# Performance work log

Measured on AMD Instinct MI355X. Metric: run time of the kernel, lower is better.

## Reference

```python
import jax, jax.numpy as jnp
import numpy as np

H, B, T, DH = 16, 2, 2048, 64
MODEL_DIM = 1024


def setup_inputs() -> dict:
    key = jax.random.key(0)
    ks = jax.random.split(key, 5)
    q = jax.random.normal(ks[0], (H, B, T, DH), dtype=jnp.float32)
    k = jax.random.normal(ks[1], (H, B, T, DH), dtype=jnp.float32)
    v = jax.random.normal(ks[2], (H, B, T, DH), dtype=jnp.float32)
    Wo_w = jax.random.normal(ks[3], (MODEL_DIM, H * DH), dtype=jnp.float32) * 0.02
    Wo_b = jax.random.normal(ks[4], (MODEL_DIM,), dtype=jnp.float32) * 0.02
    return {"q": q, "k": k, "v": v, "Wo_w": Wo_w, "Wo_b": Wo_b}


def reference(q, k, v, Wo_w, Wo_b):
    # per-head scaled dot-product attention; scale uses per-head dk (=DH)
    scale = jnp.sqrt(jnp.asarray(DH, dtype=q.dtype))
    # scores: [H, B, T, T]
    scores = jnp.einsum('hbtd,hbsd->hbts', q, k) / scale
    # causal mask (additive -1e12 on strict upper triangle, matching torch code)
    mask = jnp.triu(jnp.ones((T, T), dtype=bool), 1)
    scores = scores + (-1e12) * mask.astype(scores.dtype)
    weights = jax.nn.softmax(scores, axis=-1)
    # context per head: [H, B, T, DH]
    context = jnp.einsum('hbts,hbsd->hbtd', weights, v)
    # concat heads along feature dim: [B, T, H*DH]
    context = jnp.transpose(context, (1, 2, 0, 3)).reshape(B, T, H * DH)
    # output projection (torch Linear: x @ W.T + b)
    return context @ Wo_w.T + Wo_b
```

## Files before the change

kernel.cpp:

```cpp
#include <hip/hip_runtime.h>

typedef __attribute__((ext_vector_type(8))) short bf16x8;
typedef __attribute__((ext_vector_type(4))) float f32x4;
typedef __attribute__((ext_vector_type(4))) unsigned int u32x4;
typedef __attribute__((ext_vector_type(4))) unsigned short u16x4;

#define H_ 16
#define B_ 2
#define T_ 2048
#define DH_ 64
#define MD_ 1024

static __device__ inline unsigned short f2bf(float f) {
    union { float f; unsigned u; } x; x.f = f;
    unsigned r = (x.u + 0x7fffu + ((x.u >> 16) & 1u)) >> 16;
    return (unsigned short)r;
}
static __device__ inline unsigned int pack_bf2(float lo, float hi) {
    return __builtin_amdgcn_perm(__float_as_uint(hi), __float_as_uint(lo), 0x07060302u);
}
static __device__ inline unsigned short hi16(float f) {
    return (unsigned short)(__float_as_uint(f) >> 16);
}

__global__ __launch_bounds__(256) void prep_k(const float* __restrict__ k,
                                              const float* __restrict__ v,
                                              const float* __restrict__ w,
                                              unsigned short* __restrict__ kb,
                                              unsigned short* __restrict__ vtb,
                                              unsigned short* __restrict__ wob) {
    __shared__ __attribute__((aligned(16))) unsigned short vt64[64][64];
    const int blk = blockIdx.x;
    const int tid = threadIdx.x;
    if (blk < 1024) {
        int i = (blk * 256 + tid) * 4;
        f32x4 x = *(const f32x4*)(w + i);
        u16x4 y;
        y[0] = f2bf(x[0]); y[1] = f2bf(x[1]); y[2] = f2bf(x[2]); y[3] = f2bf(x[3]);
        *(u16x4*)(wob + i) = y;
    } else if (blk < 2048) {
        int j = blk - 1024;
        const int hb = j >> 5, s0 = (j & 31) * 64;
        const int row = tid >> 2, c = (tid & 3) * 16;
        const long off = (long)hb * (T_ * DH_) + (long)(s0 + row) * DH_ + c;
        const float* p = k + off;
        f32x4 a0 = *(const f32x4*)p;
        f32x4 a1 = *(const f32x4*)(p + 4);
        f32x4 a2 = *(const f32x4*)(p + 8);
        f32x4 a3 = *(const f32x4*)(p + 12);
        u32x4 w0, w1;
        w0[0] = pack_bf2(a0[0], a0[1]); w0[1] = pack_bf2(a0[2], a0[3]);
        w0[2] = pack_bf2(a1[0], a1[1]); w0[3] = pack_bf2(a1[2], a1[3]);
        w1[0] = pack_bf2(a2[0], a2[1]); w1[1] = pack_bf2(a2[2], a2[3]);
        w1[2] = pack_bf2(a3[0], a3[1]); w1[3] = pack_bf2(a3[2], a3[3]);
        *(u32x4*)(kb + off) = w0;
        *(u32x4*)(kb + off + 8) = w1;
    } else {
        int j = blk - 2048;
        const int hb = j >> 5, s0 = (j & 31) * 64;
        const int vkp = tid & 31, vdg = tid >> 5;
        const float* vp = v + (long)hb * (T_ * DH_) + (long)(s0 + 2 * vkp) * DH_ + vdg * 8;
        f32x4 va0 = *(const f32x4*)vp;
        f32x4 va1 = *(const f32x4*)(vp + 4);
        f32x4 vb0 = *(const f32x4*)(vp + DH_);
        f32x4 vb1 = *(const f32x4*)(vp + DH_ + 4);
#pragma unroll
        for (int jj = 0; jj < 4; jj++) {
            ((unsigned int*)&vt64[vdg * 8 + jj][0])[vkp]     = pack_bf2(va0[jj], vb0[jj]);
            ((unsigned int*)&vt64[vdg * 8 + 4 + jj][0])[vkp] = pack_bf2(va1[jj], vb1[jj]);
        }
        __syncthreads();
        const int dh = tid >> 2, kc = (tid & 3) * 16;
        u32x4 o0 = *(const u32x4*)&vt64[dh][kc];
        u32x4 o1 = *(const u32x4*)&vt64[dh][kc + 8];
        unsigned short* op = vtb + (long)hb * (DH_ * T_) + (long)dh * T_ + s0 + kc;
        *(u32x4*)op = o0;
        *(u32x4*)(op + 8) = o1;
    }
}

__global__ __launch_bounds__(256, 4) void attn_k(const float* __restrict__ q,
                                                 const unsigned short* __restrict__ kb,
                                                 const unsigned short* __restrict__ vtb,
                                                 unsigned short* __restrict__ ctx) {
    const int i = blockIdx.x;
    const int xcd = i & 7, j = i >> 3;
    const int cu = j & 31, l = j >> 5;
    const int hb = xcd * 4 + l;
    const int t = (l & 1) ? (31 - cu) : cu;
    const int h = hb >> 1, b = hb & 1;
    const int tid = threadIdx.x;
    const int wave = tid >> 6, lane = tid & 63;
    const int ln = lane & 15, quad = lane >> 4;

    __shared__ __attribute__((aligned(16))) unsigned short kt[64][72];
    __shared__ __attribute__((aligned(16))) unsigned short vt[64][72];
    __shared__ __attribute__((aligned(16))) unsigned short pl[4][16][72];

    const long kbase = (long)hb * (T_ * DH_);
    const long vbase = (long)hb * (DH_ * T_);
    const int nsteps = t + 1;
    const int q0w = t * 64 + wave * 16;
    const int srow = tid >> 2, sc = (tid & 3) * 16;

    bf16x8 ones;
#pragma unroll
    for (int z = 0; z < 8; z++) ones[z] = (short)0x3F80;

    bf16x8 qf0, qf1;
    {
        const float* qp = q + kbase + (long)(q0w + ln) * DH_ + quad * 8;
        f32x4 a0 = *(const f32x4*)qp;
        f32x4 a1 = *(const f32x4*)(qp + 4);
        f32x4 b0 = *(const f32x4*)(qp + 32);
        f32x4 b1 = *(const f32x4*)(qp + 36);
#pragma unroll
        for (int z = 0; z < 4; z++) {
            qf0[z]   = (short)f2bf(a0[z] * 0.125f);
            qf0[4+z] = (short)f2bf(a1[z] * 0.125f);
            qf1[z]   = (short)f2bf(b0[z] * 0.125f);
            qf1[4+z] = (short)f2bf(b1[z] * 0.125f);
        }
    }

    f32x4 oacc[4];
#pragma unroll
    for (int z = 0; z < 4; z++) oacc[z] = f32x4{0.f, 0.f, 0.f, 0.f};
    f32x4 lacc = f32x4{0.f, 0.f, 0.f, 0.f};

    u32x4 kr0, kr1, vr0, vr1;
    {
        const unsigned short* kp = kb + kbase + (long)srow * DH_ + sc;
        kr0 = *(const u32x4*)kp; kr1 = *(const u32x4*)(kp + 8);
        const unsigned short* vp = vtb + vbase + (long)srow * T_ + sc;
        vr0 = *(const u32x4*)vp; vr1 = *(const u32x4*)(vp + 8);
    }

#pragma unroll 1
    for (int step = 0; step < nsteps; step++) {
        __syncthreads();
        *(u32x4*)&kt[srow][sc]     = kr0;
        *(u32x4*)&kt[srow][sc + 8] = kr1;
        *(u32x4*)&vt[srow][sc]     = vr0;
        *(u32x4*)&vt[srow][sc + 8] = vr1;
        __syncthreads();

        if (step + 1 < nsteps) {
            const unsigned short* kp = kb + kbase + (long)((step + 1) * 64 + srow) * DH_ + sc;
            kr0 = *(const u32x4*)kp; kr1 = *(const u32x4*)(kp + 8);
            const unsigned short* vp = vtb + vbase + (long)srow * T_ + (step + 1) * 64 + sc;
            vr0 = *(const u32x4*)vp; vr1 = *(const u32x4*)(vp + 8);
        }

        f32x4 sa[4];
#pragma unroll
        for (int nt = 0; nt < 4; nt++) {
            bf16x8 kf0 = *(const bf16x8*)&kt[nt * 16 + ln][quad * 8];
            bf16x8 kf1 = *(const bf16x8*)&kt[nt * 16 + ln][32 + quad * 8];
            f32x4 a = f32x4{0.f, 0.f, 0.f, 0.f};
            a = __builtin_amdgcn_mfma_f32_16x16x32_bf16(qf0, kf0, a, 0, 0, 0);
            a = __builtin_amdgcn_mfma_f32_16x16x32_bf16(qf1, kf1, a, 0, 0, 0);
            sa[nt] = a;
        }

        if (step == nsteps - 1) {
            const int lr = wave * 16 + quad * 4;
#pragma unroll
            for (int nt = 0; nt < 4; nt++)
#pragma unroll
                for (int r = 0; r < 4; r++) {
                    float p = __expf(sa[nt][r]);
                    if (nt * 16 + ln > lr + r) p = 0.f;
                    pl[wave][quad * 4 + r][nt * 16 + ln] = hi16(p);
                }
        } else {
#pragma unroll
            for (int nt = 0; nt < 4; nt++)
#pragma unroll
                for (int r = 0; r < 4; r++)
                    pl[wave][quad * 4 + r][nt * 16 + ln] = hi16(__expf(sa[nt][r]));
        }

        bf16x8 pf0 = *(const bf16x8*)&pl[wave][ln][quad * 8];
        bf16x8 pf1 = *(const bf16x8*)&pl[wave][ln][32 + quad * 8];

#pragma unroll
        for (int dt = 0; dt < 4; dt++) {
            bf16x8 vf0 = *(const bf16x8*)&vt[dt * 16 + ln][quad * 8];
            bf16x8 vf1 = *(const bf16x8*)&vt[dt * 16 + ln][32 + quad * 8];
            oacc[dt] = __builtin_amdgcn_mfma_f32_16x16x32_bf16(pf0, vf0, oacc[dt], 0, 0, 0);
            oacc[dt] = __builtin_amdgcn_mfma_f32_16x16x32_bf16(pf1, vf1, oacc[dt], 0, 0, 0);
        }
        lacc = __builtin_amdgcn_mfma_f32_16x16x32_bf16(pf0, ones, lacc, 0, 0, 0);
        lacc = __builtin_amdgcn_mfma_f32_16x16x32_bf16(pf1, ones, lacc, 0, 0, 0);
    }

#pragma unroll
    for (int r = 0; r < 4; r++) {
        float rl = __builtin_amdgcn_rcpf(lacc[r]);
        int row_g = q0w + quad * 4 + r;
#pragma unroll
        for (int dt = 0; dt < 4; dt++)
            ctx[(long)(b * T_ + row_g) * MD_ + h * 64 + dt * 16 + ln] =
                f2bf(oacc[dt][r] * rl);
    }
}

__global__ __launch_bounds__(256, 4) void proj_k(const unsigned short* __restrict__ A,
                                                 const unsigned short* __restrict__ Bw,
                                                 const float* __restrict__ bias,
                                                 float* __restrict__ out) {
    const int i = blockIdx.x;
    const int n0 = ((i & 7) * 2 + ((i >> 3) & 1)) * 64;
    const int m0 = (i >> 4) * 64;
    const int tid = threadIdx.x;
    const int wave = tid >> 6, lane = tid & 63;
    const int ln = lane & 15, quad = lane >> 4;

    __shared__ __attribute__((aligned(16))) unsigned short As[64][72];
    __shared__ __attribute__((aligned(16))) unsigned short Bs[64][72];

    const int srow = tid >> 2, sc = (tid & 3) * 16;

    f32x4 acc[4];
#pragma unroll
    for (int z = 0; z < 4; z++) acc[z] = f32x4{0.f, 0.f, 0.f, 0.f};

    u32x4 ar0, ar1, br0, br1;
    {
        const unsigned short* ap = A + (long)(m0 + srow) * 1024 + sc;
        ar0 = *(const u32x4*)ap; ar1 = *(const u32x4*)(ap + 8);
        const unsigned short* bp = Bw + (long)(n0 + srow) * 1024 + sc;
        br0 = *(const u32x4*)bp; br1 = *(const u32x4*)(bp + 8);
    }

#pragma unroll 1
    for (int ks = 0; ks < 1024; ks += 64) {
        __syncthreads();
        *(u32x4*)&As[srow][sc]     = ar0;
        *(u32x4*)&As[srow][sc + 8] = ar1;
        *(u32x4*)&Bs[srow][sc]     = br0;
        *(u32x4*)&Bs[srow][sc + 8] = br1;
        __syncthreads();

        if (ks + 64 < 1024) {
            const unsigned short* ap = A + (long)(m0 + srow) * 1024 + ks + 64 + sc;
            ar0 = *(const u32x4*)ap; ar1 = *(const u32x4*)(ap + 8);
            const unsigned short* bp = Bw + (long)(n0 + srow) * 1024 + ks + 64 + sc;
            br0 = *(const u32x4*)bp; br1 = *(const u32x4*)(bp + 8);
        }

        bf16x8 bf0 = *(const bf16x8*)&Bs[wave * 16 + ln][quad * 8];
        bf16x8 bf1 = *(const bf16x8*)&Bs[wave * 16 + ln][32 + quad * 8];
#pragma unroll
        for (int mt = 0; mt < 4; mt++) {
            bf16x8 af0 = *(const bf16x8*)&As[mt * 16 + ln][quad * 8];
            bf16x8 af1 = *(const bf16x8*)&As[mt * 16 + ln][32 + quad * 8];
            acc[mt] = __builtin_amdgcn_mfma_f32_16x16x32_bf16(af0, bf0, acc[mt], 0, 0, 0);
            acc[mt] = __builtin_amdgcn_mfma_f32_16x16x32_bf16(af1, bf1, acc[mt], 0, 0, 0);
        }
    }

    int col = n0 + wave * 16 + ln;
    float bz = bias[col];
#pragma unroll
    for (int mt = 0; mt < 4; mt++)
#pragma unroll
        for (int r = 0; r < 4; r++) {
            int row = m0 + mt * 16 + quad * 4 + r;
            out[(long)row * 1024 + col] = acc[mt][r] + bz;
        }
}

extern "C" void kernel_launch(void* const* d_in, const int* in_sizes, int n_in,
                              void* d_out, int out_size, void* d_ws, size_t ws_size,
                              hipStream_t stream) {
    const float* q    = (const float*)d_in[0];
    const float* k    = (const float*)d_in[1];
    const float* v    = (const float*)d_in[2];
    const float* Wo_w = (const float*)d_in[3];
    const float* Wo_b = (const float*)d_in[4];
    float* out = (float*)d_out;

    unsigned short* ctx = (unsigned short*)d_ws;
    unsigned short* wob = ctx + (size_t)4096 * 1024;
    unsigned short* kbb = wob + (size_t)1024 * 1024;
    unsigned short* vtb = kbb + (size_t)32 * 2048 * 64;

    prep_k<<<3072, 256, 0, stream>>>(k, v, Wo_w, kbb, vtb, wob);
    attn_k<<<1024, 256, 0, stream>>>(q, kbb, vtb, ctx);
    proj_k<<<1024, 256, 0, stream>>>(ctx, wob, Wo_b, out);
}
```

Before: 155.3 us.

## Split long causal query tiles across two blocks and merge partial results

Query tiles 16-31 are now each split into two KV ranges handled by separate blocks, following a balanced 48-entry schedule per head, so the grid grows from 1024 to 1536 blocks and per-block work is more even. Each block of a split pair writes unnormalised partial outputs and row sums to workspace. An atomic counter lets the second block to finish add both halves, normalise and write the context row. The exponential also switches to exp2 with log2(e) folded into the query scale. The split adds workspace traffic, a flag-clearing block in the prep kernel and atomics, in exchange for a shorter critical path on the longest tiles.

Result: no change. 152.5 us (-1.7%).

```diff
diff --git a/kernel.cpp b/kernel.cpp
--- a/kernel.cpp
+++ b/kernel.cpp
@@ -22,13 +22,21 @@
 static __device__ inline unsigned short hi16(float f) {
     return (unsigned short)(__float_as_uint(f) >> 16);
 }
+static __device__ inline float fexp2(float x) {
+#if __has_builtin(__builtin_amdgcn_exp2f)
+    return __builtin_amdgcn_exp2f(x);
+#else
+    return exp2f(x);
+#endif
+}
 
 __global__ __launch_bounds__(256) void prep_k(const float* __restrict__ k,
                                               const float* __restrict__ v,
                                               const float* __restrict__ w,
                                               unsigned short* __restrict__ kb,
                                               unsigned short* __restrict__ vtb,
-                                              unsigned short* __restrict__ wob) {
+                                              unsigned short* __restrict__ wob,
+                                              int* __restrict__ fl) {
     __shared__ __attribute__((aligned(16))) unsigned short vt64[64][64];
     const int blk = blockIdx.x;
     const int tid = threadIdx.x;
@@ -55,7 +63,7 @@
         w1[2] = pack_bf2(a3[0], a3[1]); w1[3] = pack_bf2(a3[2], a3[3]);
         *(u32x4*)(kb + off) = w0;
         *(u32x4*)(kb + off + 8) = w1;
-    } else {
+    } else if (blk < 3072) {
         int j = blk - 2048;
         const int hb = j >> 5, s0 = (j & 31) * 64;
         const int vkp = tid & 31, vdg = tid >> 5;
@@ -76,18 +84,40 @@
         unsigned short* op = vtb + (long)hb * (DH_ * T_) + (long)dh * T_ + s0 + kc;
         *(u32x4*)op = o0;
         *(u32x4*)(op + 8) = o1;
-    }
-}
+    } else {
+        for (int z = tid; z < 512; z += 256) fl[z] = 0;
+    }
+}
+
+#define SE(t, lo, hi) ((unsigned)((t) | ((lo) << 8) | ((hi) << 16)))
+__constant__ unsigned sched48[48] = {
+    SE(31,0,16), SE(31,16,32), SE(30,15,31), SE(15,0,16),
+    SE(30,0,15), SE(29,0,15), SE(29,15,30), SE(28,14,29), SE(14,0,15),
+    SE(28,0,14), SE(27,0,14), SE(27,14,28), SE(26,13,27), SE(13,0,14),
+    SE(26,0,13), SE(25,0,13), SE(25,13,26), SE(24,12,25), SE(12,0,13),
+    SE(24,0,12), SE(23,0,12), SE(23,12,24), SE(22,11,23), SE(11,0,12),
+    SE(22,0,11), SE(21,0,11), SE(21,11,22), SE(20,10,21), SE(10,0,11),
+    SE(20,0,10), SE(19,0,10), SE(19,10,20), SE(18,9,19), SE(9,0,10),
+    SE(18,0,9), SE(17,0,9), SE(17,9,18), SE(16,8,17), SE(8,0,9),
+    SE(16,0,8), SE(7,0,8),
+    SE(6,0,7), SE(5,0,6), SE(4,0,5), SE(3,0,4), SE(2,0,3), SE(1,0,2), SE(0,0,1)
+};
 
 __global__ __launch_bounds__(256, 4) void attn_k(const float* __restrict__ q,
                                                  const unsigned short* __restrict__ kb,
                                                  const unsigned short* __restrict__ vtb,
-                                                 unsigned short* __restrict__ ctx) {
+                                                 unsigned short* __restrict__ ctx,
+                                                 float* __restrict__ Op,
+                                                 float* __restrict__ lp,
+                                                 int* __restrict__ fl) {
     const int i = blockIdx.x;
     const int xcd = i & 7, j = i >> 3;
-    const int cu = j & 31, l = j >> 5;
+    const int l = j & 3, idx = j >> 2;
+    const unsigned e = sched48[idx];
+    const int t  = (int)(e & 255u);
+    const int lo = (int)((e >> 8) & 255u);
+    const int hi = (int)(e >> 16);
     const int hb = xcd * 4 + l;
-    const int t = (l & 1) ? (31 - cu) : cu;
     const int h = hb >> 1, b = hb & 1;
     const int tid = threadIdx.x;
     const int wave = tid >> 6, lane = tid & 63;
@@ -96,10 +126,10 @@
     __shared__ __attribute__((aligned(16))) unsigned short kt[64][72];
     __shared__ __attribute__((aligned(16))) unsigned short vt[64][72];
     __shared__ __attribute__((aligned(16))) unsigned short pl[4][16][72];
+    __shared__ int sh_who;
 
     const long kbase = (long)hb * (T_ * DH_);
     const long vbase = (long)hb * (DH_ * T_);
-    const int nsteps = t + 1;
     const int q0w = t * 64 + wave * 16;
     const int srow = tid >> 2, sc = (tid & 3) * 16;
 
@@ -109,6 +139,7 @@
 
     bf16x8 qf0, qf1;
     {
+        const float qs = 0.18033688011112042f;
         const float* qp = q + kbase + (long)(q0w + ln) * DH_ + quad * 8;
         f32x4 a0 = *(const f32x4*)qp;
         f32x4 a1 = *(const f32x4*)(qp + 4);
@@ -116,10 +147,10 @@
         f32x4 b1 = *(const f32x4*)(qp + 36);
 #pragma unroll
         for (int z = 0; z < 4; z++) {
-            qf0[z]   = (short)f2bf(a0[z] * 0.125f);
-            qf0[4+z] = (short)f2bf(a1[z] * 0.125f);
-            qf1[z]   = (short)f2bf(b0[z] * 0.125f);
-            qf1[4+z] = (short)f2bf(b1[z] * 0.125f);
+            qf0[z]   = (short)f2bf(a0[z] * qs);
+            qf0[4+z] = (short)f2bf(a1[z] * qs);
+            qf1[z]   = (short)f2bf(b0[z] * qs);
+            qf1[4+z] = (short)f2bf(b1[z] * qs);
         }
     }
 
@@ -130,14 +161,14 @@
 
     u32x4 kr0, kr1, vr0, vr1;
     {
-        const unsigned short* kp = kb + kbase + (long)srow * DH_ + sc;
+        const unsigned short* kp = kb + kbase + (long)(lo * 64 + srow) * DH_ + sc;
         kr0 = *(const u32x4*)kp; kr1 = *(const u32x4*)(kp + 8);
-        const unsigned short* vp = vtb + vbase + (long)srow * T_ + sc;
+        const unsigned short* vp = vtb + vbase + (long)srow * T_ + lo * 64 + sc;
         vr0 = *(const u32x4*)vp; vr1 = *(const u32x4*)(vp + 8);
     }
 
 #pragma unroll 1
-    for (int step = 0; step < nsteps; step++) {
+    for (int step = lo; step < hi; step++) {
         __syncthreads();
         *(u32x4*)&kt[srow][sc]     = kr0;
         *(u32x4*)&kt[srow][sc + 8] = kr1;
@@ -145,7 +176,7 @@
         *(u32x4*)&vt[srow][sc + 8] = vr1;
         __syncthreads();
 
-        if (step + 1 < nsteps) {
+        if (step + 1 < hi) {
             const unsigned short* kp = kb + kbase + (long)((step + 1) * 64 + srow) * DH_ + sc;
             kr0 = *(const u32x4*)kp; kr1 = *(const u32x4*)(kp + 8);
             const unsigned short* vp = vtb + vbase + (long)srow * T_ + (step + 1) * 64 + sc;
@@ -163,13 +194,13 @@
             sa[nt] = a;
         }
 
-        if (step == nsteps - 1) {
+        if (step == t) {
             const int lr = wave * 16 + quad * 4;
 #pragma unroll
             for (int nt = 0; nt < 4; nt++)
 #pragma unroll
                 for (int r = 0; r < 4; r++) {
-                    float p = __expf(sa[nt][r]);
+                    float p = fexp2(sa[nt][r]);
                     if (nt * 16 + ln > lr + r) p = 0.f;
                     pl[wave][quad * 4 + r][nt * 16 + ln] = hi16(p);
                 }
@@ -178,7 +209,7 @@
             for (int nt = 0; nt < 4; nt++)
 #pragma unroll
                 for (int r = 0; r < 4; r++)
-                    pl[wave][quad * 4 + r][nt * 16 + ln] = hi16(__expf(sa[nt][r]));
+                    pl[wave][quad * 4 + r][nt * 16 + ln] = hi16(fexp2(sa[nt][r]));
         }
 
         bf16x8 pf0 = *(const bf16x8*)&pl[wave][ln][quad * 8];
@@ -195,14 +226,58 @@
         lacc = __builtin_amdgcn_mfma_f32_16x16x32_bf16(pf1, ones, lacc, 0, 0, 0);
     }
 
-#pragma unroll
-    for (int r = 0; r < 4; r++) {
-        float rl = __builtin_amdgcn_rcpf(lacc[r]);
-        int row_g = q0w + quad * 4 + r;
-#pragma unroll
-        for (int dt = 0; dt < 4; dt++)
-            ctx[(long)(b * T_ + row_g) * MD_ + h * 64 + dt * 16 + ln] =
-                f2bf(oacc[dt][r] * rl);
+    if (t < 16) {
+#pragma unroll
+        for (int r = 0; r < 4; r++) {
+            float rl = __builtin_amdgcn_rcpf(lacc[r]);
+            int row_g = q0w + quad * 4 + r;
+#pragma unroll
+            for (int dt = 0; dt < 4; dt++)
+                ctx[(long)(b * T_ + row_g) * MD_ + h * 64 + dt * 16 + ln] =
+                    f2bf(oacc[dt][r] * rl);
+        }
+    } else {
+        const int c = (lo != 0) ? 1 : 0;
+        const long prow = (long)(t - 16) * 64 + wave * 16 + quad * 4;
+        const long pbase = (((long)c * 32 + hb) * 1024 + prow) * 64 + ln;
+#pragma unroll
+        for (int r = 0; r < 4; r++)
+#pragma unroll
+            for (int dt = 0; dt < 4; dt++)
+                __hip_atomic_store(&Op[pbase + (long)r * 64 + dt * 16], oacc[dt][r],
+                                   __ATOMIC_RELAXED, __HIP_MEMORY_SCOPE_AGENT);
+        if (ln == 0) {
+#pragma unroll
+            for (int r = 0; r < 4; r++)
+                __hip_atomic_store(&lp[((long)c * 32 + hb) * 1024 + prow + r], lacc[r],
+                                   __ATOMIC_RELAXED, __HIP_MEMORY_SCOPE_AGENT);
+        }
+        __syncthreads();
+        if (tid == 0)
+            sh_who = __hip_atomic_fetch_add(&fl[hb * 16 + (t - 16)], 1,
+                                            __ATOMIC_RELAXED, __HIP_MEMORY_SCOPE_AGENT);
+        __syncthreads();
+        if (sh_who == 1) {
+            const long qbase = (((long)(c ^ 1) * 32 + hb) * 1024 + prow) * 64 + ln;
+#pragma unroll
+            for (int r = 0; r < 4; r++) {
+#pragma unroll
+                for (int dt = 0; dt < 4; dt++)
+                    oacc[dt][r] += __hip_atomic_load(&Op[qbase + (long)r * 64 + dt * 16],
+                                                     __ATOMIC_RELAXED, __HIP_MEMORY_SCOPE_AGENT);
+                lacc[r] += __hip_atomic_load(&lp[((long)(c ^ 1) * 32 + hb) * 1024 + prow + r],
+                                             __ATOMIC_RELAXED, __HIP_MEMORY_SCOPE_AGENT);
+            }
+#pragma unroll
+            for (int r = 0; r < 4; r++) {
+                float rl = __builtin_amdgcn_rcpf(lacc[r]);
+                int row_g = q0w + quad * 4 + r;
+#pragma unroll
+                for (int dt = 0; dt < 4; dt++)
+                    ctx[(long)(b * T_ + row_g) * MD_ + h * 64 + dt * 16 + ln] =
+                        f2bf(oacc[dt][r] * rl);
+            }
+        }
     }
 }
 
@@ -286,8 +361,11 @@
     unsigned short* wob = ctx + (size_t)4096 * 1024;
     unsigned short* kbb = wob + (size_t)1024 * 1024;
     unsigned short* vtb = kbb + (size_t)32 * 2048 * 64;
-
-    prep_k<<<3072, 256, 0, stream>>>(k, v, Wo_w, kbb, vtb, wob);
-    attn_k<<<1024, 256, 0, stream>>>(q, kbb, vtb, ctx);
+    float* Opart = (float*)(vtb + (size_t)32 * 2048 * 64);
+    float* lpart = Opart + (size_t)2 * 32 * 1024 * 64;
+    int*   flags = (int*)(lpart + (size_t)2 * 32 * 1024);
+
+    prep_k<<<3073, 256, 0, stream>>>(k, v, Wo_w, kbb, vtb, wob, flags);
+    attn_k<<<1536, 256, 0, stream>>>(q, kbb, vtb, ctx, Opart, lpart, flags);
     proj_k<<<1024, 256, 0, stream>>>(ctx, wob, Wo_b, out);
 }
```
